# Kernel optimization log

Hardware: AMD Instinct MI355X
Metric: run time of the kernel (lower is better)

Reference implementation:

```python
import jax, jax.numpy as jnp
import numpy as np

D_MODEL = 1024
N_HEADS = 16
D_HEAD = D_MODEL // N_HEADS


def setup_inputs() -> dict:
    key = jax.random.key(0)
    ks = jax.random.split(key, 9)
    s = 1.0 / np.sqrt(D_MODEL)
    x = jax.random.normal(ks[0], (4, 2048, D_MODEL), dtype=jnp.float32)
    wq = jax.random.uniform(ks[1], (D_MODEL, D_MODEL), jnp.float32, -s, s)
    wk = jax.random.uniform(ks[2], (D_MODEL, D_MODEL), jnp.float32, -s, s)
    wv = jax.random.uniform(ks[3], (D_MODEL, D_MODEL), jnp.float32, -s, s)
    wo = jax.random.uniform(ks[4], (D_MODEL, D_MODEL), jnp.float32, -s, s)
    bq = jax.random.uniform(ks[5], (D_MODEL,), jnp.float32, -s, s)
    bk = jax.random.uniform(ks[6], (D_MODEL,), jnp.float32, -s, s)
    bv = jax.random.uniform(ks[7], (D_MODEL,), jnp.float32, -s, s)
    bo = jax.random.uniform(ks[8], (D_MODEL,), jnp.float32, -s, s)
    return {"x": x, "wq": wq, "bq": bq, "wk": wk, "bk": bk,
            "wv": wv, "bv": bv, "wo": wo, "bo": bo}


def reference(x, wq, bq, wk, bk, wv, bv, wo, bo):
    B, T, D = x.shape
    H, Dh = N_HEADS, D_HEAD
    # nn.Linear: y = x @ W.T + b
    q = (x @ wq.T + bq).reshape(B, T, H, Dh).transpose(0, 2, 1, 3)  # (B,H,T,Dh)
    k = (x @ wk.T + bk).reshape(B, T, H, Dh).transpose(0, 2, 1, 3)
    v = (x @ wv.T + bv).reshape(B, T, H, Dh).transpose(0, 2, 1, 3)
    scores = jnp.einsum('bhqd,bhkd->bhqk', q, k) / jnp.sqrt(jnp.float32(Dh))
    causal_mask = jnp.triu(jnp.ones((T, T), dtype=bool), k=1)  # True above diag
    scores = jnp.where(causal_mask[None, None], jnp.float32(-jnp.inf), scores)
    attn = jax.nn.softmax(scores, axis=-1)  # dropout p=0.0 -> identity
    out = jnp.einsum('bhqk,bhkd->bhqd', attn, v)
    out = out.transpose(0, 2, 1, 3).reshape(B, T, D)
    return out @ wo.T + bo
```

## Files before the change

### kernel.cpp

```cpp
#include <hip/hip_runtime.h>

typedef __bf16 bf16x8 __attribute__((ext_vector_type(8)));
typedef float f32x4 __attribute__((ext_vector_type(4)));
typedef float f32x16 __attribute__((ext_vector_type(16)));
typedef unsigned short u16;
typedef unsigned int u32;

#define DEV static __device__ __forceinline__

DEV u16 f2bf(float f) {
  u32 u = __builtin_bit_cast(u32, f);
  u += 0x7fffu + ((u >> 16) & 1u);
  return (u16)(u >> 16);
}

DEV f32x4 mfma16(bf16x8 a, bf16x8 b, f32x4 c) {
  return __builtin_amdgcn_mfma_f32_16x16x32_bf16(a, b, c, 0, 0, 0);
}

DEV f32x16 mfma32(bf16x8 a, bf16x8 b, f32x16 c) {
  return __builtin_amdgcn_mfma_f32_32x32x16_bf16(a, b, c, 0, 0, 0);
}

DEV u32 cvtpk(float lo, float hi) {
  u32 r;
  asm("v_cvt_pk_bf16_f32 %0, %1, %2" : "=v"(r) : "v"(lo), "v"(hi));
  return r;
}

DEV void gload16(const void* g, void* l) {
  __builtin_amdgcn_global_load_lds((const __attribute__((address_space(1))) u32*)g,
                                   (__attribute__((address_space(3))) u32*)l, 16, 0, 0);
}

__global__ void pack_w(const float* __restrict__ wq, const float* __restrict__ wk,
                       const float* __restrict__ wv, const float* __restrict__ wo,
                       const float* __restrict__ bq, const float* __restrict__ bk,
                       const float* __restrict__ bv,
                       u16* __restrict__ Wqkv, u16* __restrict__ Wo, float* __restrict__ bqkv) {
  const int i = blockIdx.x * 256 + threadIdx.x;
  if (i < 3145728) {
    const int n = i >> 10;
    const float* s = (n < 1024) ? wq : (n < 2048) ? wk : wv;
    Wqkv[i] = f2bf(s[(n & 1023) * 1024 + (i & 1023)]);
  } else if (i < 4194304) {
    Wo[i - 3145728] = f2bf(wo[i - 3145728]);
  } else if (i < 4197376) {
    const int j = i - 4194304;
    bqkv[j] = (j < 1024) ? bq[j] : (j < 2048) ? bk[j - 1024] : bv[j - 2048];
  }
}

__global__ void cvt_x(const float4* __restrict__ x, u16* __restrict__ xb) {
  const int i = blockIdx.x * 256 + threadIdx.x;
  float4 v = x[i];
  union { u16 h[4]; uint2 d; } r;
  r.h[0] = f2bf(v.x); r.h[1] = f2bf(v.y); r.h[2] = f2bf(v.z); r.h[3] = f2bf(v.w);
  *(uint2*)&xb[(size_t)i * 4] = r.d;
}

template<int MODE>
__global__ __launch_bounds__(256)
void gemm_bt(const u16* __restrict__ A, const u16* __restrict__ B,
             const float* __restrict__ bias, float* __restrict__ Cf,
             u16* __restrict__ Qs, u16* __restrict__ Ks, u16* __restrict__ Vts,
             int K) {
  __shared__ u16 Asm[128 * 32];
  __shared__ u16 Bsm[128 * 32];
  const int tid = threadIdx.x, lane = tid & 63, w = tid >> 6;
  const int tn = blockIdx.x, tm = blockIdx.y;
  const int wr = w >> 1, wc = w & 1;
  f32x4 acc[4][4] = {};
  const size_t Kb = (size_t)K * 2;
  const char* Ab = (const char*)A + (size_t)(tm * 128) * Kb;
  const char* Bb = (const char*)B + (size_t)(tn * 128) * Kb;
  const int c0 = w * 2, c1 = c0 + 1;
  const size_t soff0 = (size_t)(c0 * 16 + (lane >> 2)) * Kb + (size_t)(lane & 3) * 16;
  const size_t soff1 = (size_t)(c1 * 16 + (lane >> 2)) * Kb + (size_t)(lane & 3) * 16;
  u16* la0 = Asm + c0 * 512;  u16* la1 = Asm + c1 * 512;
  u16* lb0 = Bsm + c0 * 512;  u16* lb1 = Bsm + c1 * 512;
  const int ar = (wr * 64 + (lane & 15)) * 32 + (lane >> 4) * 8;
  const int br = (wc * 64 + (lane & 15)) * 32 + (lane >> 4) * 8;

  for (int kt = 0; kt < K; kt += 32) {
    if (kt) __syncthreads();
    gload16(Ab + soff0 + (size_t)kt * 2, la0);
    gload16(Ab + soff1 + (size_t)kt * 2, la1);
    gload16(Bb + soff0 + (size_t)kt * 2, lb0);
    gload16(Bb + soff1 + (size_t)kt * 2, lb1);
    __syncthreads();
    bf16x8 af[4], bfv[4];
#pragma unroll
    for (int mf = 0; mf < 4; mf++) af[mf] = *(const bf16x8*)&Asm[ar + mf * 512];
#pragma unroll
    for (int nf = 0; nf < 4; nf++) bfv[nf] = *(const bf16x8*)&Bsm[br + nf * 512];
#pragma unroll
    for (int mf = 0; mf < 4; mf++)
#pragma unroll
      for (int nf = 0; nf < 4; nf++)
        acc[mf][nf] = mfma16(af[mf], bfv[nf], acc[mf][nf]);
  }

  const int nbase = tn * 128 + wc * 64 + (lane & 15);
  const int mbase = tm * 128 + wr * 64 + (lane >> 4) * 4;
  const float SCQ = 0.18033688011112042f;
#pragma unroll
  for (int nf = 0; nf < 4; nf++) {
    const int n = nbase + nf * 16;
    const float bias_n = bias[n];
    if (MODE == 0) {
      const int sec = n >> 10;
      const int h = (n & 1023) >> 6, dh = n & 63;
#pragma unroll
      for (int mf = 0; mf < 4; mf++) {
#pragma unroll
        for (int r = 0; r < 4; r++) {
          const int m = mbase + mf * 16 + r;
          const int b = m >> 11, t = m & 2047;
          const size_t base = (size_t)(b * 16 + h) << 17;
          const float vv = acc[mf][nf][r] + bias_n;
          if (sec == 0)      Qs[base + (size_t)t * 64 + dh] = f2bf(vv * SCQ);
          else if (sec == 1) Ks[base + (size_t)t * 64 + dh] = f2bf(vv);
          else               Vts[base + (size_t)dh * 2048 + t] = f2bf(vv);
        }
      }
    } else {
#pragma unroll
      for (int mf = 0; mf < 4; mf++)
#pragma unroll
        for (int r = 0; r < 4; r++) {
          const int m = mbase + mf * 16 + r;
          Cf[(size_t)m * 1024 + n] = acc[mf][nf][r] + bias_n;
        }
    }
  }
}

__global__ __launch_bounds__(256, 4)
void attn32(const u16* __restrict__ Qg, const u16* __restrict__ Kg,
            const u16* __restrict__ Vt, u16* __restrict__ AO) {
  const int lane = threadIdx.x & 63, w = threadIdx.x >> 6;
  const int bh = blockIdx.x;
  const int yy = blockIdx.y;
  const int gq = yy >> 2, oq = yy & 3;
  const int qt = (gq == 0) ? oq : (gq == 1) ? 15 - oq : (gq == 2) ? 4 + oq : 11 - oq;
  const int l31 = lane & 31, h = lane >> 5;
  const int q0 = qt * 128 + w * 32;
  const size_t hb = (size_t)bh << 17;

  bf16x8 qf[4];
  const u16* qrow_p = Qg + hb + (size_t)(q0 + l31) * 64 + h * 8;
#pragma unroll
  for (int s = 0; s < 4; s++) qf[s] = *(const bf16x8*)(qrow_p + s * 16);

  f32x16 o0 = {}, o1 = {};
  float m = -3.0e38f, lr = 0.f;

  const u16* kp  = Kg + hb + (size_t)l31 * 64 + h * 8;
  const u16* vp0 = Vt + hb + (size_t)l31 * 2048 + h * 8;
  const u16* vp1 = vp0 + 32 * 2048;

  bf16x8 kA[4], kB[4];
#pragma unroll
  for (int j = 0; j < 4; j++) kA[j] = *(const bf16x8*)(kp + j * 16);

  auto step = [&](bf16x8 (&kc)[4], bf16x8 (&kn)[4], int kb) {
    bf16x8 vc0 = *(const bf16x8*)(vp0 + kb);
    bf16x8 vc1 = *(const bf16x8*)(vp0 + kb + 16);
    bf16x8 vc2 = *(const bf16x8*)(vp1 + kb);
    bf16x8 vc3 = *(const bf16x8*)(vp1 + kb + 16);

    f32x16 sa = {};
    __builtin_amdgcn_s_setprio(1);
    sa = mfma32(kc[0], qf[0], sa);
    sa = mfma32(kc[1], qf[1], sa);
    sa = mfma32(kc[2], qf[2], sa);
    sa = mfma32(kc[3], qf[3], sa);
    __builtin_amdgcn_s_setprio(0);

    if (kb + 32 <= q0) {
      const u16* kt2 = kp + (size_t)(kb + 32) * 64;
#pragma unroll
      for (int j = 0; j < 4; j++) kn[j] = *(const bf16x8*)(kt2 + j * 16);
    }

    if (kb == q0) {
#pragma unroll
      for (int r = 0; r < 16; r++) {
        const int kl = (r & 3) + 8 * (r >> 2) + 4 * h;
        if (kl > l31) sa[r] = -3.0e38f;
      }
    }

    float pmax = fmaxf(sa[0], sa[1]);
#pragma unroll
    for (int r = 2; r < 16; r++) pmax = fmaxf(pmax, sa[r]);
    pmax = fmaxf(pmax, __shfl_xor(pmax, 32));

    if (!__all(pmax - m <= 8.0f)) {
      const float mn = fmaxf(m, pmax);
      const float al = exp2f(m - mn);
      lr *= al;
#pragma unroll
      for (int r = 0; r < 16; r++) { o0[r] *= al; o1[r] *= al; }
      m = mn;
    }

    u32 W[8];
    float rs = 0.f;
#pragma unroll
    for (int j = 0; j < 8; j++) {
      const float e0 = exp2f(sa[2 * j] - m);
      const float e1 = exp2f(sa[2 * j + 1] - m);
      rs += e0 + e1;
      W[j] = cvtpk(e0, e1);
    }
    rs += __shfl_xor(rs, 32);
    lr += rs;

    asm volatile("v_permlane32_swap_b32 %0, %1" : "+v"(W[0]), "+v"(W[2]));
    asm volatile("v_permlane32_swap_b32 %0, %1" : "+v"(W[1]), "+v"(W[3]));
    asm volatile("v_permlane32_swap_b32 %0, %1" : "+v"(W[4]), "+v"(W[6]));
    asm volatile("v_permlane32_swap_b32 %0, %1" : "+v"(W[5]), "+v"(W[7]));
    union { u32 u[4]; bf16x8 v; } f0, f1;
    f0.u[0] = W[0]; f0.u[1] = W[1]; f0.u[2] = W[2]; f0.u[3] = W[3];
    f1.u[0] = W[4]; f1.u[1] = W[5]; f1.u[2] = W[6]; f1.u[3] = W[7];

    __builtin_amdgcn_s_setprio(1);
    o0 = mfma32(vc0, f0.v, o0);
    o0 = mfma32(vc1, f1.v, o0);
    o1 = mfma32(vc2, f0.v, o1);
    o1 = mfma32(vc3, f1.v, o1);
    __builtin_amdgcn_s_setprio(0);
  };

  int kb = 0;
  for (;;) {
    step(kA, kB, kb);
    kb += 32; if (kb > q0) break;
    step(kB, kA, kb);
    kb += 32; if (kb > q0) break;
  }

  const float inv = 1.0f / lr;
  const int b = bh >> 4, hh = bh & 15;
  const int q = q0 + l31;
  u16* orow = AO + (size_t)(b * 2048 + q) * 1024 + hh * 64;
#pragma unroll
  for (int r = 0; r < 16; r += 2) {
    const int dh = (r & 3) + 8 * (r >> 2) + 4 * h;
    *(u32*)(orow + dh)      = cvtpk(o0[r] * inv, o0[r + 1] * inv);
    *(u32*)(orow + 32 + dh) = cvtpk(o1[r] * inv, o1[r + 1] * inv);
  }
}

extern "C" void kernel_launch(void* const* d_in, const int* in_sizes, int n_in,
                              void* d_out, int out_size, void* d_ws, size_t ws_size,
                              hipStream_t stream) {
  const float* x  = (const float*)d_in[0];
  const float* wq = (const float*)d_in[1];
  const float* bq = (const float*)d_in[2];
  const float* wk = (const float*)d_in[3];
  const float* bk = (const float*)d_in[4];
  const float* wv = (const float*)d_in[5];
  const float* bv = (const float*)d_in[6];
  const float* wo = (const float*)d_in[7];
  const float* bo = (const float*)d_in[8];

  char* p = (char*)d_ws;
  u16* xb    = (u16*)p;   p += 16777216;
  u16* Wqkv  = (u16*)p;   p += 6291456;
  u16* Wo    = (u16*)p;   p += 2097152;
  float* bqkv = (float*)p; p += 12288;
  u16* Qs    = (u16*)p;   p += 16777216;
  u16* Ks    = (u16*)p;   p += 16777216;
  u16* Vts   = (u16*)p;   p += 16777216;
  u16* AO    = xb;

  pack_w<<<16396, 256, 0, stream>>>(wq, wk, wv, wo, bq, bk, bv, Wqkv, Wo, bqkv);
  cvt_x<<<8192, 256, 0, stream>>>((const float4*)x, xb);
  gemm_bt<0><<<dim3(24, 64), 256, 0, stream>>>(xb, Wqkv, bqkv, nullptr, Qs, Ks, Vts, 1024);
  attn32<<<dim3(64, 16), 256, 0, stream>>>(Qs, Ks, Vts, AO);
  gemm_bt<1><<<dim3(8, 64), 256, 0, stream>>>(AO, Wo, bo, (float*)d_out,
                                              nullptr, nullptr, nullptr, 1024);
}
```

Before: 367.0 us.

## Use single-wave attention blocks in longest-first order and permlane32 swap reductions

The attention kernel changes from 256-thread blocks, each covering a 128-row query tile over 4 waves, to 64-thread single-wave blocks, each covering a 32-row query tile. Query tiles are launched longest-first (63 - blockIdx.y) so the causal workload balances better across CUs. The half-wave max and sum reductions and the P-fragment lane swaps now use the permlane32_swap builtin instead of __shfl_xor (a DS-based shuffle) and inline asm. This lets the compiler schedule those instructions, at the cost of more blocks and lost cross-wave L2/cache locality within a block.

```diff
diff --git a/kernel.cpp b/kernel.cpp
--- a/kernel.cpp
+++ b/kernel.cpp
@@ -5,8 +5,16 @@
 typedef float f32x16 __attribute__((ext_vector_type(16)));
 typedef unsigned short u16;
 typedef unsigned int u32;
+typedef unsigned int u32x2 __attribute__((ext_vector_type(2)));
 
 #define DEV static __device__ __forceinline__
+
+#if __has_builtin(__builtin_amdgcn_permlane32_swap)
+#define PLSWAP_BUILTIN 1
+#endif
+
+DEV u32 f2u(float f) { return __builtin_bit_cast(u32, f); }
+DEV float u2f(u32 u) { return __builtin_bit_cast(float, u); }
 
 DEV u16 f2bf(float f) {
   u32 u = __builtin_bit_cast(u32, f);
@@ -26,6 +34,23 @@
   u32 r;
   asm("v_cvt_pk_bf16_f32 %0, %1, %2" : "=v"(r) : "v"(lo), "v"(hi));
   return r;
+}
+
+DEV float hred_max(float x) {
+#ifdef PLSWAP_BUILTIN
+  u32x2 r = __builtin_amdgcn_permlane32_swap(f2u(x), f2u(x), false, false);
+  return fmaxf(u2f(r.x), u2f(r.y));
+#else
+  return fmaxf(x, __shfl_xor(x, 32));
+#endif
+}
+DEV float hred_add(float x) {
+#ifdef PLSWAP_BUILTIN
+  u32x2 r = __builtin_amdgcn_permlane32_swap(f2u(x), f2u(x), false, false);
+  return u2f(r.x) + u2f(r.y);
+#else
+  return x + __shfl_xor(x, 32);
+#endif
 }
 
 DEV void gload16(const void* g, void* l) {
@@ -136,16 +161,14 @@
   }
 }
 
-__global__ __launch_bounds__(256, 4)
+__global__ __launch_bounds__(64, 4)
 void attn32(const u16* __restrict__ Qg, const u16* __restrict__ Kg,
             const u16* __restrict__ Vt, u16* __restrict__ AO) {
-  const int lane = threadIdx.x & 63, w = threadIdx.x >> 6;
+  const int lane = threadIdx.x;
   const int bh = blockIdx.x;
-  const int yy = blockIdx.y;
-  const int gq = yy >> 2, oq = yy & 3;
-  const int qt = (gq == 0) ? oq : (gq == 1) ? 15 - oq : (gq == 2) ? 4 + oq : 11 - oq;
+  const int qi = 63 - (int)blockIdx.y;
   const int l31 = lane & 31, h = lane >> 5;
-  const int q0 = qt * 128 + w * 32;
+  const int q0 = qi * 32;
   const size_t hb = (size_t)bh << 17;
 
   bf16x8 qf[4];
@@ -195,7 +218,7 @@
     float pmax = fmaxf(sa[0], sa[1]);
 #pragma unroll
     for (int r = 2; r < 16; r++) pmax = fmaxf(pmax, sa[r]);
-    pmax = fmaxf(pmax, __shfl_xor(pmax, 32));
+    pmax = hred_max(pmax);
 
     if (!__all(pmax - m <= 8.0f)) {
       const float mn = fmaxf(m, pmax);
@@ -215,16 +238,26 @@
       rs += e0 + e1;
       W[j] = cvtpk(e0, e1);
     }
-    rs += __shfl_xor(rs, 32);
-    lr += rs;
-
+    lr += hred_add(rs);
+
+    union { u32 u[4]; bf16x8 v; } f0, f1;
+#ifdef PLSWAP_BUILTIN
+    {
+      u32x2 r02 = __builtin_amdgcn_permlane32_swap(W[0], W[2], false, false);
+      u32x2 r13 = __builtin_amdgcn_permlane32_swap(W[1], W[3], false, false);
+      u32x2 r46 = __builtin_amdgcn_permlane32_swap(W[4], W[6], false, false);
+      u32x2 r57 = __builtin_amdgcn_permlane32_swap(W[5], W[7], false, false);
+      f0.u[0] = r02.x; f0.u[1] = r13.x; f0.u[2] = r02.y; f0.u[3] = r13.y;
+      f1.u[0] = r46.x; f1.u[1] = r57.x; f1.u[2] = r46.y; f1.u[3] = r57.y;
+    }
+#else
     asm volatile("v_permlane32_swap_b32 %0, %1" : "+v"(W[0]), "+v"(W[2]));
     asm volatile("v_permlane32_swap_b32 %0, %1" : "+v"(W[1]), "+v"(W[3]));
     asm volatile("v_permlane32_swap_b32 %0, %1" : "+v"(W[4]), "+v"(W[6]));
     asm volatile("v_permlane32_swap_b32 %0, %1" : "+v"(W[5]), "+v"(W[7]));
-    union { u32 u[4]; bf16x8 v; } f0, f1;
     f0.u[0] = W[0]; f0.u[1] = W[1]; f0.u[2] = W[2]; f0.u[3] = W[3];
     f1.u[0] = W[4]; f1.u[1] = W[5]; f1.u[2] = W[6]; f1.u[3] = W[7];
+#endif
 
     __builtin_amdgcn_s_setprio(1);
     o0 = mfma32(vc0, f0.v, o0);
@@ -280,7 +313,7 @@
   pack_w<<<16396, 256, 0, stream>>>(wq, wk, wv, wo, bq, bk, bv, Wqkv, Wo, bqkv);
   cvt_x<<<8192, 256, 0, stream>>>((const float4*)x, xb);
   gemm_bt<0><<<dim3(24, 64), 256, 0, stream>>>(xb, Wqkv, bqkv, nullptr, Qs, Ks, Vts, 1024);
-  attn32<<<dim3(64, 16), 256, 0, stream>>>(Qs, Ks, Vts, AO);
+  attn32<<<dim3(64, 64), 64, 0, stream>>>(Qs, Ks, Vts, AO);
   gemm_bt<1><<<dim3(8, 64), 256, 0, stream>>>(AO, Wo, bo, (float*)d_out,
                                               nullptr, nullptr, nullptr, 1024);
 }
```

New measurement: 353.9 us. -3.6%, faster.
